# Kernel optimization log

Hardware: AMD Instinct MI355X
Metric: run time of the kernel (lower is better)

The kernel has to match this reference:

```python
import jax, jax.numpy as jnp
import numpy as np

BN_EPS = 1e-3  # O-CNN default bn_eps


def setup_inputs() -> dict:
    key = jax.random.key(0)
    k1, k2, k3 = jax.random.split(key, 3)
    N, Cin, Cout, K = 100000, 32, 32, 27  # nodes, channels, 3x3x3 taps
    data_in = jax.random.normal(k1, (1, Cin, N, 1), dtype=jnp.float32)
    neigh = jax.random.randint(k2, (N, K), 0, N, dtype=jnp.int32)
    weight = jax.random.normal(k3, (K, Cin, Cout), dtype=jnp.float32) * 0.05
    gamma = jnp.ones((Cout,), dtype=jnp.float32)
    beta = jnp.zeros((Cout,), dtype=jnp.float32)
    return {"data_in": data_in, "neigh": neigh, "weight": weight,
            "gamma": gamma, "beta": beta}


def reference(data_in, neigh, weight, gamma, beta):
    # data_in: [1, Cin, N, 1] -> x: [N, Cin]
    x = data_in[0, :, :, 0].T
    # Octree conv: gather 27 neighbor features per node, then small matmul.
    col = x[neigh]                                   # [N, 27, Cin] (irregular gather)
    y = jnp.einsum('nkc,kcd->nd', col, weight)       # [N, Cout]
    # BatchNorm2d in training mode: stats over the N (spatial) axis.
    mean = jnp.mean(y, axis=0)
    var = jnp.mean(jnp.square(y - mean), axis=0)     # biased variance, as BN uses
    yn = (y - mean) * jax.lax.rsqrt(var + BN_EPS) * gamma + beta
    # back to O-CNN layout [1, Cout, N, 1]
    return yn.T[None, :, :, None]
```

## Files before the change

### kernel.cpp

```cpp
#include <hip/hip_runtime.h>

#define KK 27

typedef short bf16x8 __attribute__((ext_vector_type(8)));
typedef float f32x4  __attribute__((ext_vector_type(4)));

__device__ inline unsigned short f2bf(float f) {
    unsigned u = __float_as_uint(f);
    unsigned r = u + 0x7fffu + ((u >> 16) & 1u);
    return (unsigned short)(r >> 16);
}

__global__ __launch_bounds__(256) void xprep_k(const float* __restrict__ in,
                                               unsigned short* __restrict__ xTb, int N) {
    __shared__ float tile[32][33];
    int n0 = blockIdx.x * 32;
    int tx = threadIdx.x & 31;
    int ty = threadIdx.x >> 5;
#pragma unroll
    for (int c = ty; c < 32; c += 8) {
        int n = n0 + tx;
        tile[c][tx] = (n < N) ? in[(long)c * N + n] : 0.f;
    }
    __syncthreads();
#pragma unroll
    for (int nn = ty; nn < 32; nn += 8) {
        int n = n0 + nn;
        if (n < N) xTb[(long)n * 32 + tx] = f2bf(tile[tx][nn]);
    }
}

__global__ __launch_bounds__(256) void wprep_k(const float* __restrict__ w,
                                               unsigned short* __restrict__ wTb) {
    int k = blockIdx.x;
    for (int i = threadIdx.x; i < 1024; i += 256) {
        int cin = i >> 5, cout = i & 31;
        wTb[k * 1024 + cout * 32 + cin] = f2bf(w[k * 1024 + cin * 32 + cout]);
    }
}

__global__ __launch_bounds__(64, 4) void conv_k(const unsigned short* __restrict__ xTb,
                                                const int* __restrict__ neigh,
                                                const unsigned short* __restrict__ wTb,
                                                float* __restrict__ y,
                                                float* __restrict__ partial,
                                                int N, int nrows) {
    __shared__ float ct[32][33];

    const int L    = threadIdx.x;
    const int r16  = L & 15;
    const int quad = L >> 4;
    const int base = blockIdx.x * 32;
    const int n0 = base + r16;
    const int n1 = base + 16 + r16;
    const bool v0 = (n0 < N), v1 = (n1 < N);
    const long nb0 = (long)(v0 ? n0 : 0) * KK;
    const long nb1 = (long)(v1 ? n1 : 0) * KK;

    const bf16x8 zz = {0, 0, 0, 0, 0, 0, 0, 0};

    f32x4 acc00 = {0.f, 0.f, 0.f, 0.f};
    f32x4 acc01 = acc00, acc10 = acc00, acc11 = acc00;

    int ia = neigh[nb0];
    int ib = neigh[nb1];
    int ja = neigh[nb0 + 1];
    int jb = neigh[nb1 + 1];

    bf16x8 a0 = *(const bf16x8*)(xTb + (long)ia * 32 + quad * 8);
    bf16x8 a1 = *(const bf16x8*)(xTb + (long)ib * 32 + quad * 8);
    bf16x8 b0 = *(const bf16x8*)(wTb + r16 * 32 + quad * 8);
    bf16x8 b1 = *(const bf16x8*)(wTb + (16 + r16) * 32 + quad * 8);
    a0 = v0 ? a0 : zz;
    a1 = v1 ? a1 : zz;

#pragma unroll 1
    for (int k = 0; k < KK; ++k) {
        bf16x8 na0 = zz, na1 = zz, pb0 = zz, pb1 = zz;
        if (k < KK - 1) {
            na0 = *(const bf16x8*)(xTb + (long)ja * 32 + quad * 8);
            na1 = *(const bf16x8*)(xTb + (long)jb * 32 + quad * 8);
            const unsigned short* wn = wTb + (k + 1) * 1024;
            pb0 = *(const bf16x8*)(wn + r16 * 32 + quad * 8);
            pb1 = *(const bf16x8*)(wn + (16 + r16) * 32 + quad * 8);
            int kk = (k + 2 < KK) ? (k + 2) : (KK - 1);
            ja = neigh[nb0 + kk];
            jb = neigh[nb1 + kk];
        }

        acc00 = __builtin_amdgcn_mfma_f32_16x16x32_bf16(a0, b0, acc00, 0, 0, 0);
        acc01 = __builtin_amdgcn_mfma_f32_16x16x32_bf16(a0, b1, acc01, 0, 0, 0);
        acc10 = __builtin_amdgcn_mfma_f32_16x16x32_bf16(a1, b0, acc10, 0, 0, 0);
        acc11 = __builtin_amdgcn_mfma_f32_16x16x32_bf16(a1, b1, acc11, 0, 0, 0);

        if (k < KK - 1) {
            a0 = v0 ? na0 : zz;
            a1 = v1 ? na1 : zz;
            b0 = pb0;
            b1 = pb1;
        }
    }

    float s0 = 0.f, q0 = 0.f, s1 = 0.f, q1 = 0.f;
#pragma unroll
    for (int r = 0; r < 4; ++r) {
        s0 += acc00[r] + acc10[r];
        q0 += acc00[r] * acc00[r] + acc10[r] * acc10[r];
        s1 += acc01[r] + acc11[r];
        q1 += acc01[r] * acc01[r] + acc11[r] * acc11[r];
    }
#pragma unroll
    for (int off = 16; off < 64; off <<= 1) {
        s0 += __shfl_xor(s0, off, 64);
        q0 += __shfl_xor(q0, off, 64);
        s1 += __shfl_xor(s1, off, 64);
        q1 += __shfl_xor(q1, off, 64);
    }
    if (L < 16) {
        const int b = blockIdx.x;
        partial[(long)L * nrows + b]        = s0;
        partial[(long)(L + 16) * nrows + b] = s1;
        partial[(long)(L + 32) * nrows + b] = q0;
        partial[(long)(L + 48) * nrows + b] = q1;
    }

#pragma unroll
    for (int r = 0; r < 4; ++r) {
        ct[quad * 4 + r][r16]           = acc00[r];
        ct[quad * 4 + r][16 + r16]      = acc01[r];
        ct[16 + quad * 4 + r][r16]      = acc10[r];
        ct[16 + quad * 4 + r][16 + r16] = acc11[r];
    }
    __syncthreads();
    const int node = L & 31;
    const int half = L >> 5;
    const int gn = base + node;
#pragma unroll
    for (int i = 0; i < 16; ++i) {
        const int cout = i * 2 + half;
        if (gn < N) y[(long)cout * N + gn] = ct[node][cout];
    }
}

__global__ __launch_bounds__(256) void stats1_k(const float* __restrict__ partial,
                                                int nrows, float* __restrict__ tot) {
    __shared__ float red[256];
    const int col = blockIdx.x;
    const float* row = partial + (long)col * nrows;
    float s = 0.f;
    for (int r = threadIdx.x; r < nrows; r += 256) s += row[r];
    red[threadIdx.x] = s;
    __syncthreads();
    for (int w = 128; w >= 64; w >>= 1) {
        if (threadIdx.x < w) red[threadIdx.x] += red[threadIdx.x + w];
        __syncthreads();
    }
    if (threadIdx.x < 64) {
        float v = red[threadIdx.x];
#pragma unroll
        for (int off = 1; off < 64; off <<= 1) v += __shfl_xor(v, off, 64);
        if (threadIdx.x == 0) tot[col] = v;
    }
}

__global__ __launch_bounds__(256) void norm_k(float* __restrict__ y,
                                              const float* __restrict__ tot,
                                              const float* __restrict__ gamma,
                                              const float* __restrict__ beta, int N) {
    const int d = blockIdx.y;
    const float mean = tot[d] / (float)N;
    const float var  = tot[d + 32] / (float)N - mean * mean;
    const float sc   = gamma[d] * rsqrtf(var + 1e-3f);
    const float sh   = beta[d] - mean * sc;

    int i = blockIdx.x * blockDim.x + threadIdx.x;
    int base = i * 4;
    if (base + 3 < N) {
        float4* p = (float4*)(y + (long)d * N + base);
        float4 v = *p;
        v.x = fmaf(v.x, sc, sh);
        v.y = fmaf(v.y, sc, sh);
        v.z = fmaf(v.z, sc, sh);
        v.w = fmaf(v.w, sc, sh);
        *p = v;
    } else if (base < N) {
        for (int t = base; t < N; ++t) y[(long)d * N + t] = fmaf(y[(long)d * N + t], sc, sh);
    }
}

extern "C" void kernel_launch(void* const* d_in, const int* in_sizes, int n_in,
                              void* d_out, int out_size, void* d_ws, size_t ws_size,
                              hipStream_t stream) {
    const float* data_in = (const float*)d_in[0];
    const int*   neigh   = (const int*)d_in[1];
    const float* weight  = (const float*)d_in[2];
    const float* gamma   = (const float*)d_in[3];
    const float* beta    = (const float*)d_in[4];
    float* out = (float*)d_out;

    const int N = in_sizes[1] / KK;
    const int nblk  = (N + 31) / 32;
    const int nrows = nblk;

    char* ws = (char*)d_ws;
    unsigned short* xTb = (unsigned short*)ws;
    unsigned short* wTb = (unsigned short*)(ws + (size_t)N * 64);
    float* partial = (float*)(ws + (size_t)N * 64 + 55296);
    float* tot     = partial + (size_t)64 * nrows;

    xprep_k<<<nblk, 256, 0, stream>>>(data_in, xTb, N);
    wprep_k<<<KK, 256, 0, stream>>>(weight, wTb);
    conv_k<<<nblk, 64, 0, stream>>>(xTb, neigh, wTb, out, partial, N, nrows);
    stats1_k<<<64, 256, 0, stream>>>(partial, nrows, tot);
    dim3 ngrid(((N + 3) / 4 + 255) / 256, 32);
    norm_k<<<ngrid, 256, 0, stream>>>(out, tot, gamma, beta, N);
}
```

Measured before the change: 138.3 us.

## Split conv taps across waves, fuse prep kernels, atomic BN stats

The conv kernel now uses 256-thread blocks. Each pair of waves splits the 27 taps (14 and 13), and the partial accumulators are combined through shared memory. This adds latency hiding with a 3-deep software prefetch, and invalid rows are pointed at a zeroed padding row of xTb. The x and w prep kernels are merged into one launch, and the separate stats-reduction kernel is replaced by per-block atomicAdd into a memset total, cutting launches. The costs are more shared memory and syncs per block, and atomic contention on 64 addresses.

```diff
diff --git a/kernel.cpp b/kernel.cpp
--- a/kernel.cpp
+++ b/kernel.cpp
@@ -11,155 +11,187 @@
     return (unsigned short)(r >> 16);
 }
 
-__global__ __launch_bounds__(256) void xprep_k(const float* __restrict__ in,
-                                               unsigned short* __restrict__ xTb, int N) {
+__global__ __launch_bounds__(256) void prep_k(const float* __restrict__ in,
+                                              const float* __restrict__ w,
+                                              unsigned short* __restrict__ xTb,
+                                              unsigned short* __restrict__ wTb,
+                                              int N, int nxblk) {
     __shared__ float tile[32][33];
-    int n0 = blockIdx.x * 32;
-    int tx = threadIdx.x & 31;
-    int ty = threadIdx.x >> 5;
-#pragma unroll
-    for (int c = ty; c < 32; c += 8) {
-        int n = n0 + tx;
-        tile[c][tx] = (n < N) ? in[(long)c * N + n] : 0.f;
-    }
-    __syncthreads();
-#pragma unroll
-    for (int nn = ty; nn < 32; nn += 8) {
-        int n = n0 + nn;
-        if (n < N) xTb[(long)n * 32 + tx] = f2bf(tile[tx][nn]);
-    }
-}
-
-__global__ __launch_bounds__(256) void wprep_k(const float* __restrict__ w,
-                                               unsigned short* __restrict__ wTb) {
-    int k = blockIdx.x;
-    for (int i = threadIdx.x; i < 1024; i += 256) {
-        int cin = i >> 5, cout = i & 31;
-        wTb[k * 1024 + cout * 32 + cin] = f2bf(w[k * 1024 + cin * 32 + cout]);
-    }
-}
-
-__global__ __launch_bounds__(64, 4) void conv_k(const unsigned short* __restrict__ xTb,
-                                                const int* __restrict__ neigh,
-                                                const unsigned short* __restrict__ wTb,
-                                                float* __restrict__ y,
-                                                float* __restrict__ partial,
-                                                int N, int nrows) {
-    __shared__ float ct[32][33];
-
-    const int L    = threadIdx.x;
-    const int r16  = L & 15;
-    const int quad = L >> 4;
-    const int base = blockIdx.x * 32;
+    const int b = blockIdx.x;
+    if (b < nxblk) {
+        int n0 = b * 32;
+        int tx = threadIdx.x & 31;
+        int ty = threadIdx.x >> 5;
+#pragma unroll
+        for (int c = ty; c < 32; c += 8) {
+            int n = n0 + tx;
+            tile[c][tx] = (n < N) ? in[(long)c * N + n] : 0.f;
+        }
+        __syncthreads();
+#pragma unroll
+        for (int nn = ty; nn < 32; nn += 8) {
+            int n = n0 + nn;
+            if (n < N) xTb[(long)n * 32 + tx] = f2bf(tile[tx][nn]);
+        }
+        if (b == 0 && threadIdx.x < 32) xTb[(long)N * 32 + threadIdx.x] = 0;
+    } else {
+        int k = b - nxblk;
+        for (int i = threadIdx.x; i < 1024; i += 256) {
+            int cin = i >> 5, cout = i & 31;
+            wTb[k * 1024 + cout * 32 + cin] = f2bf(w[k * 1024 + cin * 32 + cout]);
+        }
+    }
+}
+
+template <int CNT>
+__device__ __forceinline__ void conv_taps(int k0,
+                                          const unsigned short* __restrict__ xTb,
+                                          const int* __restrict__ neigh,
+                                          const unsigned short* __restrict__ wTb,
+                                          long nb0, long nb1, bool v0, bool v1,
+                                          int r16, int quad, int N,
+                                          f32x4& acc00, f32x4& acc01,
+                                          f32x4& acc10, f32x4& acc11) {
+    bf16x8 A0[3], A1[3], B0[3], B1[3];
+    int ja[3], jb[3];
+
+#pragma unroll
+    for (int d = 0; d < 3; ++d) {
+        int kk = k0 + (d < CNT ? d : CNT - 1);
+        ja[d] = v0 ? neigh[nb0 + kk] : N;
+        jb[d] = v1 ? neigh[nb1 + kk] : N;
+    }
+#pragma unroll
+    for (int d = 0; d < 3; ++d) {
+        int kk = k0 + (d < CNT ? d : CNT - 1);
+        A0[d] = *(const bf16x8*)(xTb + (long)ja[d] * 32 + quad * 8);
+        A1[d] = *(const bf16x8*)(xTb + (long)jb[d] * 32 + quad * 8);
+        const unsigned short* wn = wTb + kk * 1024;
+        B0[d] = *(const bf16x8*)(wn + r16 * 32 + quad * 8);
+        B1[d] = *(const bf16x8*)(wn + (16 + r16) * 32 + quad * 8);
+        int k2 = k0 + (d + 3 < CNT ? d + 3 : CNT - 1);
+        ja[d] = v0 ? neigh[nb0 + k2] : N;
+        jb[d] = v1 ? neigh[nb1 + k2] : N;
+    }
+#pragma unroll
+    for (int t = 0; t < CNT; ++t) {
+        const int cur = t % 3;
+        acc00 = __builtin_amdgcn_mfma_f32_16x16x32_bf16(A0[cur], B0[cur], acc00, 0, 0, 0);
+        acc01 = __builtin_amdgcn_mfma_f32_16x16x32_bf16(A0[cur], B1[cur], acc01, 0, 0, 0);
+        acc10 = __builtin_amdgcn_mfma_f32_16x16x32_bf16(A1[cur], B0[cur], acc10, 0, 0, 0);
+        acc11 = __builtin_amdgcn_mfma_f32_16x16x32_bf16(A1[cur], B1[cur], acc11, 0, 0, 0);
+        if (t + 3 < CNT) {
+            const int kk = k0 + t + 3;
+            A0[cur] = *(const bf16x8*)(xTb + (long)ja[cur] * 32 + quad * 8);
+            A1[cur] = *(const bf16x8*)(xTb + (long)jb[cur] * 32 + quad * 8);
+            const unsigned short* wn = wTb + kk * 1024;
+            B0[cur] = *(const bf16x8*)(wn + r16 * 32 + quad * 8);
+            B1[cur] = *(const bf16x8*)(wn + (16 + r16) * 32 + quad * 8);
+            const int k2 = k0 + (t + 6 < CNT ? t + 6 : CNT - 1);
+            ja[cur] = v0 ? neigh[nb0 + k2] : N;
+            jb[cur] = v1 ? neigh[nb1 + k2] : N;
+        }
+    }
+}
+
+__global__ __launch_bounds__(256, 4) void conv_k(const unsigned short* __restrict__ xTb,
+                                                 const int* __restrict__ neigh,
+                                                 const unsigned short* __restrict__ wTb,
+                                                 float* __restrict__ y,
+                                                 float* __restrict__ tot,
+                                                 int N) {
+    __shared__ float cmb[2][16][64];
+    __shared__ float ct[2][32][33];
+    __shared__ float pr[4][16];
+
+    const int tid   = threadIdx.x;
+    const int L     = tid & 63;
+    const int w     = tid >> 6;
+    const int gi    = w >> 1;
+    const int khalf = w & 1;
+    const int r16   = L & 15;
+    const int quad  = L >> 4;
+    const int base  = blockIdx.x * 64 + gi * 32;
     const int n0 = base + r16;
     const int n1 = base + 16 + r16;
     const bool v0 = (n0 < N), v1 = (n1 < N);
     const long nb0 = (long)(v0 ? n0 : 0) * KK;
     const long nb1 = (long)(v1 ? n1 : 0) * KK;
 
-    const bf16x8 zz = {0, 0, 0, 0, 0, 0, 0, 0};
-
     f32x4 acc00 = {0.f, 0.f, 0.f, 0.f};
     f32x4 acc01 = acc00, acc10 = acc00, acc11 = acc00;
 
-    int ia = neigh[nb0];
-    int ib = neigh[nb1];
-    int ja = neigh[nb0 + 1];
-    int jb = neigh[nb1 + 1];
-
-    bf16x8 a0 = *(const bf16x8*)(xTb + (long)ia * 32 + quad * 8);
-    bf16x8 a1 = *(const bf16x8*)(xTb + (long)ib * 32 + quad * 8);
-    bf16x8 b0 = *(const bf16x8*)(wTb + r16 * 32 + quad * 8);
-    bf16x8 b1 = *(const bf16x8*)(wTb + (16 + r16) * 32 + quad * 8);
-    a0 = v0 ? a0 : zz;
-    a1 = v1 ? a1 : zz;
-
-#pragma unroll 1
-    for (int k = 0; k < KK; ++k) {
-        bf16x8 na0 = zz, na1 = zz, pb0 = zz, pb1 = zz;
-        if (k < KK - 1) {
-            na0 = *(const bf16x8*)(xTb + (long)ja * 32 + quad * 8);
-            na1 = *(const bf16x8*)(xTb + (long)jb * 32 + quad * 8);
-            const unsigned short* wn = wTb + (k + 1) * 1024;
-            pb0 = *(const bf16x8*)(wn + r16 * 32 + quad * 8);
-            pb1 = *(const bf16x8*)(wn + (16 + r16) * 32 + quad * 8);
-            int kk = (k + 2 < KK) ? (k + 2) : (KK - 1);
-            ja = neigh[nb0 + kk];
-            jb = neigh[nb1 + kk];
-        }
-
-        acc00 = __builtin_amdgcn_mfma_f32_16x16x32_bf16(a0, b0, acc00, 0, 0, 0);
-        acc01 = __builtin_amdgcn_mfma_f32_16x16x32_bf16(a0, b1, acc01, 0, 0, 0);
-        acc10 = __builtin_amdgcn_mfma_f32_16x16x32_bf16(a1, b0, acc10, 0, 0, 0);
-        acc11 = __builtin_amdgcn_mfma_f32_16x16x32_bf16(a1, b1, acc11, 0, 0, 0);
-
-        if (k < KK - 1) {
-            a0 = v0 ? na0 : zz;
-            a1 = v1 ? na1 : zz;
-            b0 = pb0;
-            b1 = pb1;
-        }
-    }
+    if (khalf == 0)
+        conv_taps<14>(0,  xTb, neigh, wTb, nb0, nb1, v0, v1, r16, quad, N,
+                      acc00, acc01, acc10, acc11);
+    else
+        conv_taps<13>(14, xTb, neigh, wTb, nb0, nb1, v0, v1, r16, quad, N,
+                      acc00, acc01, acc10, acc11);
+
+    if (khalf == 1) {
+#pragma unroll
+        for (int r = 0; r < 4; ++r) {
+            cmb[gi][r][L]      = acc00[r];
+            cmb[gi][4 + r][L]  = acc01[r];
+            cmb[gi][8 + r][L]  = acc10[r];
+            cmb[gi][12 + r][L] = acc11[r];
+        }
+    }
+    __syncthreads();
 
     float s0 = 0.f, q0 = 0.f, s1 = 0.f, q1 = 0.f;
-#pragma unroll
-    for (int r = 0; r < 4; ++r) {
-        s0 += acc00[r] + acc10[r];
-        q0 += acc00[r] * acc00[r] + acc10[r] * acc10[r];
-        s1 += acc01[r] + acc11[r];
-        q1 += acc01[r] * acc01[r] + acc11[r] * acc11[r];
-    }
-#pragma unroll
-    for (int off = 16; off < 64; off <<= 1) {
-        s0 += __shfl_xor(s0, off, 64);
-        q0 += __shfl_xor(q0, off, 64);
-        s1 += __shfl_xor(s1, off, 64);
-        q1 += __shfl_xor(q1, off, 64);
-    }
-    if (L < 16) {
-        const int b = blockIdx.x;
-        partial[(long)L * nrows + b]        = s0;
-        partial[(long)(L + 16) * nrows + b] = s1;
-        partial[(long)(L + 32) * nrows + b] = q0;
-        partial[(long)(L + 48) * nrows + b] = q1;
-    }
-
-#pragma unroll
-    for (int r = 0; r < 4; ++r) {
-        ct[quad * 4 + r][r16]           = acc00[r];
-        ct[quad * 4 + r][16 + r16]      = acc01[r];
-        ct[16 + quad * 4 + r][r16]      = acc10[r];
-        ct[16 + quad * 4 + r][16 + r16] = acc11[r];
+    if (khalf == 0) {
+#pragma unroll
+        for (int r = 0; r < 4; ++r) {
+            acc00[r] += cmb[gi][r][L];
+            acc01[r] += cmb[gi][4 + r][L];
+            acc10[r] += cmb[gi][8 + r][L];
+            acc11[r] += cmb[gi][12 + r][L];
+        }
+
+#pragma unroll
+        for (int r = 0; r < 4; ++r) {
+            s0 += acc00[r] + acc10[r];
+            q0 += acc00[r] * acc00[r] + acc10[r] * acc10[r];
+            s1 += acc01[r] + acc11[r];
+            q1 += acc01[r] * acc01[r] + acc11[r] * acc11[r];
+        }
+#pragma unroll
+        for (int off = 16; off < 64; off <<= 1) {
+            s0 += __shfl_xor(s0, off, 64);
+            q0 += __shfl_xor(q0, off, 64);
+            s1 += __shfl_xor(s1, off, 64);
+            q1 += __shfl_xor(q1, off, 64);
+        }
+        if (w == 2 && L < 16) {
+            pr[0][L] = s0; pr[1][L] = s1; pr[2][L] = q0; pr[3][L] = q1;
+        }
+
+#pragma unroll
+        for (int r = 0; r < 4; ++r) {
+            ct[gi][quad * 4 + r][r16]           = acc00[r];
+            ct[gi][quad * 4 + r][16 + r16]      = acc01[r];
+            ct[gi][16 + quad * 4 + r][r16]      = acc10[r];
+            ct[gi][16 + quad * 4 + r][16 + r16] = acc11[r];
+        }
     }
     __syncthreads();
-    const int node = L & 31;
-    const int half = L >> 5;
-    const int gn = base + node;
-#pragma unroll
-    for (int i = 0; i < 16; ++i) {
-        const int cout = i * 2 + half;
-        if (gn < N) y[(long)cout * N + gn] = ct[node][cout];
-    }
-}
-
-__global__ __launch_bounds__(256) void stats1_k(const float* __restrict__ partial,
-                                                int nrows, float* __restrict__ tot) {
-    __shared__ float red[256];
-    const int col = blockIdx.x;
-    const float* row = partial + (long)col * nrows;
-    float s = 0.f;
-    for (int r = threadIdx.x; r < nrows; r += 256) s += row[r];
-    red[threadIdx.x] = s;
-    __syncthreads();
-    for (int w = 128; w >= 64; w >>= 1) {
-        if (threadIdx.x < w) red[threadIdx.x] += red[threadIdx.x + w];
-        __syncthreads();
-    }
-    if (threadIdx.x < 64) {
-        float v = red[threadIdx.x];
-#pragma unroll
-        for (int off = 1; off < 64; off <<= 1) v += __shfl_xor(v, off, 64);
-        if (threadIdx.x == 0) tot[col] = v;
+
+    if (w == 0 && L < 16) {
+        atomicAdd(&tot[L],      s0 + pr[0][L]);
+        atomicAdd(&tot[L + 16], s1 + pr[1][L]);
+        atomicAdd(&tot[L + 32], q0 + pr[2][L]);
+        atomicAdd(&tot[L + 48], q1 + pr[3][L]);
+    }
+
+    const int node = tid & 63;
+    const int gn = blockIdx.x * 64 + node;
+    if (gn < N) {
+#pragma unroll
+        for (int i = 0; i < 8; ++i) {
+            const int cout = (tid >> 6) * 8 + i;
+            y[(long)cout * N + gn] = ct[node >> 5][node & 31][cout];
+        }
     }
 }
 
@@ -199,19 +231,17 @@
     float* out = (float*)d_out;
 
     const int N = in_sizes[1] / KK;
-    const int nblk  = (N + 31) / 32;
-    const int nrows = nblk;
+    const int nxblk  = (N + 31) / 32;
+    const int nblk64 = (N + 63) / 64;
 
     char* ws = (char*)d_ws;
     unsigned short* xTb = (unsigned short*)ws;
-    unsigned short* wTb = (unsigned short*)(ws + (size_t)N * 64);
-    float* partial = (float*)(ws + (size_t)N * 64 + 55296);
-    float* tot     = partial + (size_t)64 * nrows;
-
-    xprep_k<<<nblk, 256, 0, stream>>>(data_in, xTb, N);
-    wprep_k<<<KK, 256, 0, stream>>>(weight, wTb);
-    conv_k<<<nblk, 64, 0, stream>>>(xTb, neigh, wTb, out, partial, N, nrows);
-    stats1_k<<<64, 256, 0, stream>>>(partial, nrows, tot);
+    unsigned short* wTb = (unsigned short*)(ws + (size_t)(N + 1) * 64);
+    float* tot = (float*)(ws + (size_t)(N + 1) * 64 + 55296);
+
+    hipMemsetAsync(tot, 0, 64 * sizeof(float), stream);
+    prep_k<<<nxblk + KK, 256, 0, stream>>>(data_in, weight, xTb, wTb, N, nxblk);
+    conv_k<<<nblk64, 256, 0, stream>>>(xTb, neigh, wTb, out, tot, N);
     dim3 ngrid(((N + 3) / 4 + 255) / 256, 32);
     norm_k<<<ngrid, 256, 0, stream>>>(out, tot, gamma, beta, N);
 }
```

New measurement: 151.9 us. 9.8% more time.
